# Kernel tuning notes

Hardware: AMD Instinct MI355X
Metric: run time of the kernel (lower is better)

Reference implementation:

```python
import jax, jax.numpy as jnp
import numpy as np

N_NODES = 32768
N_EDGES = 196608
N_GRAPHS = 256
DEG = 6
HID = 128
RVD = 16
EMB = HID - RVD   # atom/bond embedding dim = hidden - random_vec_dim
VOCAB = 128
TGT = 256
DEPTH = 5
N_AGG = 4         # mean, max, min, std
N_SC = 3          # identity, amplification, attenuation
EPS = 1e-5


def setup_inputs() -> dict:
    key = jax.random.key(0)
    ks = jax.random.split(key, 12)

    def g(i, shape, scale=0.05):
        return jax.random.normal(ks[i], shape, dtype=jnp.float32) * scale

    return {
        "atom_feats": jax.random.randint(ks[0], (N_NODES, 9), 0, 100),
        "bond_feats": jax.random.randint(ks[1], (N_EDGES, 3), 0, 4),
        "src": jax.random.randint(ks[2], (N_EDGES,), 0, N_NODES),
        # every node receives exactly DEG messages (DGL reduce requires in-edges)
        "dst": jnp.repeat(jnp.arange(N_NODES), DEG),
        "graph_ids": jnp.repeat(jnp.arange(N_GRAPHS), N_NODES // N_GRAPHS),
        "n_graphs": N_GRAPHS,
        "rand_x": jax.random.normal(ks[3], (N_NODES, RVD), dtype=jnp.float32),   # std=1.0
        "rand_edge": jax.random.normal(ks[4], (N_EDGES, RVD), dtype=jnp.float32),
        "atom_emb": g(5, (9, VOCAB, EMB)),
        "bond_emb": g(6, (3, VOCAB, EMB)),
        "pre_W": g(7, (DEPTH, 3 * HID, HID)),
        "pre_b": jnp.zeros((DEPTH, HID), jnp.float32),
        "post_W": g(8, (DEPTH, (N_AGG * N_SC + 1) * HID, HID)),
        "post_b": jnp.zeros((DEPTH, HID), jnp.float32),
        "ro_W1": g(9, (3 * HID, HID)),
        "ro_b1": jnp.zeros((HID,), jnp.float32),
        "ro_W2": g(10, (HID, TGT)),
        "ro_b2": jnp.zeros((TGT,), jnp.float32),
    }


def reference(atom_feats, bond_feats, src, dst, graph_ids, n_graphs,
              rand_x, rand_edge, atom_emb, bond_emb,
              pre_W, pre_b, post_W, post_b, ro_W1, ro_b1, ro_W2, ro_b2):
    n = atom_feats.shape[0]
    # OGB-style encoders: sum of per-column embeddings, then concat random vec
    h = jnp.concatenate([atom_emb[jnp.arange(9), atom_feats].sum(1), rand_x], -1)   # [N, HID]
    ef = jnp.concatenate([bond_emb[jnp.arange(3), bond_feats].sum(1), rand_edge], -1)  # [E, HID]

    deg = jax.ops.segment_sum(jnp.ones((dst.shape[0],), h.dtype), dst, n)
    degc = jnp.maximum(deg, 1.0)[:, None]
    logD = jnp.log(deg + 1.0)[:, None]                 # avg_d['log'] = 1.0
    inv_logD = jnp.where(logD > 0, 1.0 / jnp.maximum(logD, EPS), 0.0)

    def layer(hc, p):
        pW, pb, qW, qb = p
        # pretrans MLP on [src_feat, dst_feat, edge_feat]; last_activation = activation (relu)
        z = jnp.concatenate([hc[src], hc[dst], ef], -1)          # [E, 3*HID]
        e = jax.nn.relu(z @ pW + pb)                             # [E, HID]
        s = jax.ops.segment_sum(e, dst, n)
        mean = s / degc
        mean_sq = jax.ops.segment_sum(e * e, dst, n) / degc
        mx = jax.ops.segment_max(e, dst, n)
        mn = jax.ops.segment_min(e, dst, n)
        std = jnp.sqrt(jax.nn.relu(mean_sq - mean * mean) + EPS)
        agg = jnp.concatenate([mean, mx, mn, std], -1)           # [N, 4*HID]
        scaled = jnp.concatenate([agg, agg * logD, agg * inv_logD], -1)  # [N, 12*HID]
        h_new = jnp.concatenate([hc, scaled], -1) @ qW + qb + hc  # posttrans (linear) + residual
        return h_new, None

    h, _ = jax.lax.scan(layer, h, (pre_W, pre_b, post_W, post_b))

    # multi-aggregator readout: mean, sum, max per graph
    cnt = jnp.maximum(jax.ops.segment_sum(jnp.ones((n,), h.dtype), graph_ids, n_graphs), 1.0)[:, None]
    gsum = jax.ops.segment_sum(h, graph_ids, n_graphs)
    gmax = jax.ops.segment_max(h, graph_ids, n_graphs)
    r = jnp.concatenate([gsum / cnt, gsum, gmax], -1)            # [G, 3*HID]
    return jax.nn.relu(r @ ro_W1 + ro_b1) @ ro_W2 + ro_b2        # [G, TGT]
```

## Files before the change

### kernel.cpp

```cpp
#include <hip/hip_runtime.h>
#include <hip/hip_bf16.h>

#define N_NODES 32768
#define N_EDGES 196608
#define N_GRAPHS 256
#define DEG 6
#define HID 128
#define RVD 16
#define EMB 112
#define VOCAB 128
#define TGT 256
#define DEPTH 5

#define LOG7 1.9459101090932196f
#define ILOG7 0.5138983423697507f

typedef __hip_bfloat16 bf16;
using frag_ab = __attribute__((ext_vector_type(8))) short;
using frag_cd = __attribute__((ext_vector_type(4))) float;

static __device__ __forceinline__ float b2f(bf16 x) { return __bfloat162float(x); }
static __device__ __forceinline__ bf16  f2b(float x) { return __float2bfloat16(x); }
static __device__ __forceinline__ short f2s(float x) {
    bf16 b = __float2bfloat16(x);
    return *reinterpret_cast<short*>(&b);
}
static __device__ __forceinline__ float us2f(unsigned short u) {
    unsigned int x = ((unsigned int)u) << 16;
    return __uint_as_float(x);
}
static __device__ __forceinline__ unsigned short f2us(float x) {
    bf16 b = __float2bfloat16(x);
    return *reinterpret_cast<unsigned short*>(&b);
}

#define PB_ENC  16384
#define PB_WB   (PB_ENC + 640)
#define PB_WC   (PB_WB + 1600)
#define PB_WR   (PB_WC + 80)
#define PB_CODE (PB_WR + 768)
#define PB_T    (PB_CODE + 320)

__global__ __launch_bounds__(256) void prep_k(const int* __restrict__ af, const float* __restrict__ rx,
                                              const float* __restrict__ aemb, bf16* __restrict__ h,
                                              const float* __restrict__ preW, const float* __restrict__ preB,
                                              const float* __restrict__ postW,
                                              const int* __restrict__ bfeat, const float* __restrict__ bemb,
                                              bf16* __restrict__ wb, bf16* __restrict__ wc,
                                              bf16* __restrict__ wrB, unsigned char* __restrict__ codeA,
                                              bf16* __restrict__ Tb) {
    int blk = blockIdx.x, tid = threadIdx.x;
    if (blk < PB_ENC) {
        int v = blk * 2 + (tid >> 7), c = tid & 127;
        float val;
        if (c < EMB) {
            val = 0.f;
            #pragma unroll
            for (int i = 0; i < 9; ++i) {
                int f = af[v * 9 + i];
                val += aemb[(i * VOCAB + f) * EMB + c];
            }
        } else {
            val = rx[v * RVD + (c - EMB)];
        }
        h[(size_t)v * HID + c] = f2b(val);
    } else if (blk < PB_WB) {
        int idx = (blk - PB_ENC) * 256 + tid;
        if (idx < DEPTH * 32768) {
            int j = idx & 7, L = (idx >> 3) & 63, nt = (idx >> 9) & 15, ks = (idx >> 13) & 3, l = idx >> 15;
            int k = ks * 32 + ((L >> 4) * 8) + j;
            int n = nt * 16 + (L & 15);
            const float* W = preW + (size_t)l * 384 * 128;
            float v = (n < 128) ? W[k * 128 + n] : W[(128 + k) * 128 + (n - 128)];
            wb[idx] = f2b(v);
        }
    } else if (blk < PB_WC) {
        int idx = (blk - PB_WB) * 256 + tid;
        if (idx < DEPTH * 81920) {
            int j = idx & 7, L = (idx >> 3) & 63, nt = (idx >> 9) & 7;
            int t = idx >> 12;
            int ks = t % 20, l = t / 20;
            int k = ks * 32 + ((L >> 4) * 8) + j;
            int n = nt * 16 + (L & 15);
            const float* W = postW + (size_t)l * 1664 * 128;
            float v;
            if (k < 128) {
                v = W[k * 128 + n];
            } else {
                int jj = k - 128;
                v = W[(128 + jj) * 128 + n] + LOG7 * W[(640 + jj) * 128 + n] + ILOG7 * W[(1152 + jj) * 128 + n];
            }
            wc[idx] = f2b(v);
        }
    } else if (blk < PB_WR) {
        int idx = (blk - PB_WC) * 256 + tid;
        if (idx < DEPTH * 4096) {
            int j = idx & 7, L = (idx >> 3) & 63, nt = (idx >> 9) & 7, l = idx >> 12;
            int k = ((L >> 4) * 8) + j;
            int n = nt * 16 + (L & 15);
            float v = (k < 16) ? preW[(size_t)l * 384 * 128 + (368 + k) * 128 + n] : 0.f;
            wrB[idx] = f2b(v);
        }
    } else if (blk < PB_CODE) {
        int e = (blk - PB_WR) * 256 + tid;
        if (e < N_EDGES)
            codeA[e] = (unsigned char)(bfeat[e * 3] | (bfeat[e * 3 + 1] << 2) | (bfeat[e * 3 + 2] << 4));
    } else {
        if (tid < 128) {
            int t = blk - PB_CODE;
            int l = t >> 6, cd = t & 63, c = tid;
            int f0 = cd & 3, f1 = (cd >> 2) & 3, f2 = cd >> 4;
            const float* W = preW + (size_t)l * 384 * 128 + 256 * 128;
            float acc = preB[l * 128 + c];
            #pragma unroll 4
            for (int k = 0; k < EMB; ++k) {
                float bsk = bemb[(0 * VOCAB + f0) * EMB + k]
                          + bemb[(1 * VOCAB + f1) * EMB + k]
                          + bemb[(2 * VOCAB + f2) * EMB + k];
                acc += bsk * W[k * 128 + c];
            }
            Tb[(size_t)(l * 64 + cd) * 128 + c] = f2b(acc);
        }
    }
}

__global__ __launch_bounds__(256) void gemm_z12(const bf16* __restrict__ A,
                                                const bf16* __restrict__ Bp,
                                                bf16* __restrict__ C) {
    int lane = threadIdx.x & 63;
    int wave = threadIdx.x >> 6;
    int m = lane & 15, quad = lane >> 4;
    int row0 = blockIdx.x * 64 + wave * 16;

    frag_cd acc[16];
    #pragma unroll
    for (int nt = 0; nt < 16; ++nt)
        #pragma unroll
        for (int i = 0; i < 4; ++i) acc[nt][i] = 0.f;

    const frag_ab* Bf = (const frag_ab*)Bp;
    const bf16* arow = A + (size_t)(row0 + m) * 128;
    #pragma unroll
    for (int ks = 0; ks < 4; ++ks) {
        frag_ab a = *(const frag_ab*)(arow + ks * 32 + quad * 8);
        #pragma unroll
        for (int nt = 0; nt < 16; ++nt) {
            frag_ab b = Bf[(ks * 16 + nt) * 64 + lane];
            acc[nt] = __builtin_amdgcn_mfma_f32_16x16x32_bf16(a, b, acc[nt], 0, 0, 0);
        }
    }
    #pragma unroll
    for (int nt = 0; nt < 16; ++nt) {
        int col = nt * 16 + m;
        #pragma unroll
        for (int r = 0; r < 4; ++r) {
            int row = row0 + quad * 4 + r;
            C[(size_t)row * 256 + col] = f2b(acc[nt][r]);
        }
    }
}

__global__ __launch_bounds__(512) void layer_k(bf16* __restrict__ h,
                                               const bf16* __restrict__ aggc,
                                               const bf16* __restrict__ Bp,
                                               const float* __restrict__ bias,
                                               const bf16* __restrict__ Bn,
                                               bf16* __restrict__ z12) {
    __shared__ __align__(16) bf16 newh[64 * 136];
    int lane = threadIdx.x & 63;
    int wave = threadIdx.x >> 6;
    int rt = wave & 3;
    int nh = wave >> 2;
    int m = lane & 15, quad = lane >> 4;
    int row0 = blockIdx.x * 64;
    int rowA = row0 + rt * 16 + m;

    frag_cd acc[4];
    #pragma unroll
    for (int nt = 0; nt < 4; ++nt)
        #pragma unroll
        for (int i = 0; i < 4; ++i) acc[nt][i] = 0.f;

    const frag_ab* Bf = (const frag_ab*)Bp;
    const bf16* arow = h + (size_t)rowA * 128;
    #pragma unroll
    for (int ks = 0; ks < 4; ++ks) {
        frag_ab a = *(const frag_ab*)(arow + ks * 32 + quad * 8);
        #pragma unroll
        for (int nt = 0; nt < 4; ++nt) {
            frag_ab b = Bf[(ks * 8 + nh * 4 + nt) * 64 + lane];
            acc[nt] = __builtin_amdgcn_mfma_f32_16x16x32_bf16(a, b, acc[nt], 0, 0, 0);
        }
    }
    const bf16* grow = aggc + (size_t)rowA * 512;
    #pragma unroll
    for (int ks = 0; ks < 16; ++ks) {
        frag_ab a = *(const frag_ab*)(grow + ks * 32 + quad * 8);
        #pragma unroll
        for (int nt = 0; nt < 4; ++nt) {
            frag_ab b = Bf[((4 + ks) * 8 + nh * 4 + nt) * 64 + lane];
            acc[nt] = __builtin_amdgcn_mfma_f32_16x16x32_bf16(a, b, acc[nt], 0, 0, 0);
        }
    }

    __syncthreads();

    #pragma unroll
    for (int nt = 0; nt < 4; ++nt) {
        int col = nh * 64 + nt * 16 + m;
        float bs_ = bias[col];
        #pragma unroll
        for (int r = 0; r < 4; ++r) {
            int lr = rt * 16 + quad * 4 + r;
            int row = row0 + lr;
            float nv = acc[nt][r] + bs_ + b2f(h[(size_t)row * HID + col]);
            bf16 bv = f2b(nv);
            h[(size_t)row * HID + col] = bv;
            newh[lr * 136 + col] = bv;
        }
    }

    if (Bn) {
        __syncthreads();
        const frag_ab* Bf2 = (const frag_ab*)Bn;
        frag_cd a2[8];
        #pragma unroll
        for (int nt = 0; nt < 8; ++nt)
            #pragma unroll
            for (int i = 0; i < 4; ++i) a2[nt][i] = 0.f;
        #pragma unroll
        for (int ks = 0; ks < 4; ++ks) {
            frag_ab a = *(const frag_ab*)&newh[(rt * 16 + m) * 136 + ks * 32 + quad * 8];
            #pragma unroll
            for (int nt = 0; nt < 8; ++nt) {
                frag_ab b = Bf2[(ks * 16 + nh * 8 + nt) * 64 + lane];
                a2[nt] = __builtin_amdgcn_mfma_f32_16x16x32_bf16(a, b, a2[nt], 0, 0, 0);
            }
        }
        #pragma unroll
        for (int nt = 0; nt < 8; ++nt) {
            int col = nh * 128 + nt * 16 + m;
            #pragma unroll
            for (int r = 0; r < 4; ++r) {
                int row = row0 + rt * 16 + quad * 4 + r;
                z12[(size_t)row * 256 + col] = f2b(a2[nt][r]);
            }
        }
    }
}

__global__ __launch_bounds__(256) void fused_agg(const bf16* __restrict__ Z12,
                                                 const int* __restrict__ src,
                                                 const unsigned char* __restrict__ code,
                                                 const float* __restrict__ rand_edge,
                                                 const bf16* __restrict__ Tb,
                                                 const bf16* __restrict__ WrB,
                                                 bf16* __restrict__ aggc) {
    __shared__ __align__(16) float rdot[48 * 130];
    int tid = threadIdx.x;
    int lane = tid & 63, wave = tid >> 6;
    int xb = blockIdx.x & 7, tb = blockIdx.x >> 3;
    int w = xb + 8 * (tb >> 3);
    int bv = w * 64 + (tb & 7) * 8;

    if (wave < 3) {
        int m = lane & 15, quad = lane >> 4;
        frag_ab a;
        if (quad < 2) {
            const float4* rp = (const float4*)(rand_edge
                + (size_t)(bv * 6 + wave * 16 + m) * 16 + quad * 8);
            float4 A = rp[0], B = rp[1];
            a[0] = f2s(A.x); a[1] = f2s(A.y); a[2] = f2s(A.z); a[3] = f2s(A.w);
            a[4] = f2s(B.x); a[5] = f2s(B.y); a[6] = f2s(B.z); a[7] = f2s(B.w);
        } else {
            #pragma unroll
            for (int j = 0; j < 8; ++j) a[j] = 0;
        }
        const frag_ab* Bf = (const frag_ab*)WrB;
        #pragma unroll
        for (int nt = 0; nt < 8; ++nt) {
            frag_cd acc;
            #pragma unroll
            for (int i = 0; i < 4; ++i) acc[i] = 0.f;
            acc = __builtin_amdgcn_mfma_f32_16x16x32_bf16(a, Bf[nt * 64 + lane], acc, 0, 0, 0);
            #pragma unroll
            for (int r = 0; r < 4; ++r)
                rdot[(wave * 16 + quad * 4 + r) * 130 + nt * 16 + m] = acc[r];
        }
    }
    __syncthreads();

    const unsigned short* Zu = (const unsigned short*)Z12;
    const unsigned short* Tu = (const unsigned short*)Tb;
    unsigned short* Au = (unsigned short*)aggc;
    int c = lane * 2;
    int g = wave;

    #pragma unroll
    for (int i = 0; i < 2; ++i) {
        int nb = g * 2 + i;
        int v = bv + nb;
        ushort2 z2u = *(const ushort2*)(Zu + (size_t)v * 256 + 128 + c);
        float z2a = us2f(z2u.x), z2b = us2f(z2u.y);
        const int2* sp = (const int2*)(src + v * 6);
        int2 s01 = sp[0], s23 = sp[1], s45 = sp[2];
        const unsigned short* cp = (const unsigned short*)(code + v * 6);
        unsigned short c01 = cp[0], c23 = cp[1], c45 = cp[2];
        int svs[6] = { s01.x, s01.y, s23.x, s23.y, s45.x, s45.y };
        int cds[6] = { c01 & 255, c01 >> 8, c23 & 255, c23 >> 8, c45 & 255, c45 >> 8 };
        ushort2 z1u[6], tvu[6];
        #pragma unroll
        for (int j = 0; j < 6; ++j) z1u[j] = *(const ushort2*)(Zu + (size_t)svs[j] * 256 + c);
        #pragma unroll
        for (int j = 0; j < 6; ++j) tvu[j] = *(const ushort2*)(Tu + cds[j] * 128 + c);
        float sa = 0.f, ssa = 0.f, mxa = -1e30f, mna = 1e30f;
        float sb = 0.f, ssb = 0.f, mxb = -1e30f, mnb = 1e30f;
        #pragma unroll
        for (int j = 0; j < 6; ++j) {
            const float2 rd = *(const float2*)(rdot + ((nb * 6 + j) * 130) + c);
            float va = us2f(z1u[j].x) + z2a + us2f(tvu[j].x) + rd.x;
            float vb = us2f(z1u[j].y) + z2b + us2f(tvu[j].y) + rd.y;
            va = fmaxf(va, 0.f);
            vb = fmaxf(vb, 0.f);
            sa += va; ssa += va * va; mxa = fmaxf(mxa, va); mna = fminf(mna, va);
            sb += vb; ssb += vb * vb; mxb = fmaxf(mxb, vb); mnb = fminf(mnb, vb);
        }
        float meana = sa * (1.f / 6.f), meanb = sb * (1.f / 6.f);
        float msqa = ssa * (1.f / 6.f), msqb = ssb * (1.f / 6.f);
        float sda = sqrtf(fmaxf(msqa - meana * meana, 0.f) + 1e-5f);
        float sdb = sqrtf(fmaxf(msqb - meanb * meanb, 0.f) + 1e-5f);
        size_t base = (size_t)v * 512 + c;
        *(ushort2*)(Au + base)       = make_ushort2(f2us(meana), f2us(meanb));
        *(ushort2*)(Au + base + 128) = make_ushort2(f2us(mxa),  f2us(mxb));
        *(ushort2*)(Au + base + 256) = make_ushort2(f2us(mna),  f2us(mnb));
        *(ushort2*)(Au + base + 384) = make_ushort2(f2us(sda),  f2us(sdb));
    }
}

__global__ __launch_bounds__(128) void readout(const bf16* __restrict__ h, const float* __restrict__ W1,
                                               const float* __restrict__ b1, const float* __restrict__ W2,
                                               const float* __restrict__ b2, float* __restrict__ out) {
    __shared__ float r[384];
    __shared__ float y1[128];
    int g = blockIdx.x, c = threadIdx.x;
    float s = 0.f, mx = -1e30f;
    for (int v = 0; v < 128; ++v) {
        float hv = b2f(h[((size_t)g * 128 + v) * HID + c]);
        s += hv; mx = fmaxf(mx, hv);
    }
    r[c] = s * (1.f / 128.f);
    r[128 + c] = s;
    r[256 + c] = mx;
    __syncthreads();
    float a1 = b1[c];
    for (int k = 0; k < 384; ++k) a1 += r[k] * W1[k * 128 + c];
    y1[c] = fmaxf(a1, 0.f);
    __syncthreads();
    #pragma unroll
    for (int o = 0; o < 2; ++o) {
        int t = c + o * 128;
        float a2 = b2[t];
        for (int k = 0; k < 128; ++k) a2 += y1[k] * W2[k * 256 + t];
        out[(size_t)g * 256 + t] = a2;
    }
}

extern "C" void kernel_launch(void* const* d_in, const int* in_sizes, int n_in,
                              void* d_out, int out_size, void* d_ws, size_t ws_size,
                              hipStream_t stream) {
    const int*   atom_feats = (const int*)d_in[0];
    const int*   bond_feats = (const int*)d_in[1];
    const int*   src        = (const int*)d_in[2];
    const float* rand_x     = (const float*)d_in[6];
    const float* rand_edge  = (const float*)d_in[7];
    const float* atom_emb   = (const float*)d_in[8];
    const float* bond_emb   = (const float*)d_in[9];
    const float* pre_W      = (const float*)d_in[10];
    const float* pre_b      = (const float*)d_in[11];
    const float* post_W     = (const float*)d_in[12];
    const float* post_b     = (const float*)d_in[13];
    const float* ro_W1      = (const float*)d_in[14];
    const float* ro_b1      = (const float*)d_in[15];
    const float* ro_W2      = (const float*)d_in[16];
    const float* ro_b2      = (const float*)d_in[17];

    char* p = (char*)d_ws;
    auto alloc = [&](size_t bytes) {
        char* r = p;
        p += (bytes + 255) & ~(size_t)255;
        return r;
    };
    bf16*  h    = (bf16*) alloc((size_t)N_NODES * HID * 2);
    bf16*  z12  = (bf16*) alloc((size_t)N_NODES * 256 * 2);
    bf16*  aggc = (bf16*) alloc((size_t)N_NODES * 512 * 2);
    bf16*  wb   = (bf16*) alloc((size_t)DEPTH * 32768 * 2);
    bf16*  wc   = (bf16*) alloc((size_t)DEPTH * 81920 * 2);
    bf16*  wrB  = (bf16*) alloc((size_t)DEPTH * 4096 * 2);
    bf16*  Tb   = (bf16*) alloc((size_t)DEPTH * 64 * 128 * 2);
    unsigned char* code = (unsigned char*)alloc(N_EDGES);

    prep_k<<<PB_T, 256, 0, stream>>>(atom_feats, rand_x, atom_emb, h,
                                     pre_W, pre_b, post_W,
                                     bond_feats, bond_emb,
                                     wb, wc, wrB, code, Tb);

    gemm_z12<<<N_NODES / 64, 256, 0, stream>>>(h, wb, z12);

    for (int l = 0; l < DEPTH; ++l) {
        fused_agg<<<N_NODES / 8, 256, 0, stream>>>(
            z12, src, code, rand_edge,
            Tb + (size_t)l * 8192,
            wrB + (size_t)l * 4096, aggc);
        const bf16* wbn = (l + 1 < DEPTH) ? (wb + (size_t)(l + 1) * 32768) : nullptr;
        layer_k<<<N_NODES / 64, 512, 0, stream>>>(
            h, aggc, wc + (size_t)l * 81920, post_b + l * HID, wbn, z12);
    }

    readout<<<N_GRAPHS, 128, 0, stream>>>(h, ro_W1, ro_b1, ro_W2, ro_b2, (float*)d_out);
}
```

Measured before the change: 379.4 us.

## Fuse edge aggregation into layer kernel with LDS aggregates and ping-pong Z buffers

Merges the per-layer aggregation kernel and the post-transform GEMM kernel into one kernel. The 64x512 aggregate tile is kept in shared memory rather than written to and read back from a global aggc buffer, and the rdot values are stored as bf16. Z12 is double-buffered so the next layer's Z can be written while other blocks still gather the current one. This removes global aggregate traffic and one launch per layer. In exchange it adds about 80KB of LDS per block and runs aggregation serially over 8 sub-batches with barriers, which may lower occupancy and latency hiding for the gathers.

```diff
diff --git a/kernel.cpp b/kernel.cpp
--- a/kernel.cpp
+++ b/kernel.cpp
@@ -160,19 +160,101 @@
     }
 }
 
-__global__ __launch_bounds__(512) void layer_k(bf16* __restrict__ h,
-                                               const bf16* __restrict__ aggc,
-                                               const bf16* __restrict__ Bp,
-                                               const float* __restrict__ bias,
-                                               const bf16* __restrict__ Bn,
-                                               bf16* __restrict__ z12) {
-    __shared__ __align__(16) bf16 newh[64 * 136];
-    int lane = threadIdx.x & 63;
-    int wave = threadIdx.x >> 6;
-    int rt = wave & 3;
-    int nh = wave >> 2;
+__global__ __launch_bounds__(512, 4) void fused_layer(bf16* __restrict__ h,
+                                                      const bf16* __restrict__ Zcur,
+                                                      const int* __restrict__ src,
+                                                      const unsigned char* __restrict__ code,
+                                                      const float* __restrict__ rand_edge,
+                                                      const bf16* __restrict__ Tb,
+                                                      const bf16* __restrict__ WrB,
+                                                      const bf16* __restrict__ Bp,
+                                                      const float* __restrict__ bias,
+                                                      const bf16* __restrict__ Bn,
+                                                      bf16* __restrict__ Znext) {
+    __shared__ __align__(16) bf16 agg_lds[64 * 520];
+    __shared__ __align__(16) bf16 rdot[48 * 136];
+
+    int tid = threadIdx.x;
+    int lane = tid & 63, wave = tid >> 6;
     int m = lane & 15, quad = lane >> 4;
     int row0 = blockIdx.x * 64;
+
+    const unsigned short* Zu = (const unsigned short*)Zcur;
+    const unsigned short* Tu = (const unsigned short*)Tb;
+    const unsigned short* Ru = (const unsigned short*)rdot;
+    unsigned short* Ag = (unsigned short*)agg_lds;
+    int c = lane * 2;
+
+    for (int r = 0; r < 8; ++r) {
+        int bv = row0 + r * 8;
+        if (wave < 3) {
+            frag_ab a;
+            if (quad < 2) {
+                const float4* rp = (const float4*)(rand_edge
+                    + (size_t)(bv * 6 + wave * 16 + m) * 16 + quad * 8);
+                float4 A = rp[0], B = rp[1];
+                a[0] = f2s(A.x); a[1] = f2s(A.y); a[2] = f2s(A.z); a[3] = f2s(A.w);
+                a[4] = f2s(B.x); a[5] = f2s(B.y); a[6] = f2s(B.z); a[7] = f2s(B.w);
+            } else {
+                #pragma unroll
+                for (int j = 0; j < 8; ++j) a[j] = 0;
+            }
+            const frag_ab* Bf = (const frag_ab*)WrB;
+            #pragma unroll
+            for (int nt = 0; nt < 8; ++nt) {
+                frag_cd acc;
+                #pragma unroll
+                for (int i = 0; i < 4; ++i) acc[i] = 0.f;
+                acc = __builtin_amdgcn_mfma_f32_16x16x32_bf16(a, Bf[nt * 64 + lane], acc, 0, 0, 0);
+                #pragma unroll
+                for (int rr = 0; rr < 4; ++rr)
+                    rdot[(wave * 16 + quad * 4 + rr) * 136 + nt * 16 + m] = f2b(acc[rr]);
+            }
+        }
+        __syncthreads();
+        {
+            int nb = wave;
+            int v = bv + nb;
+            ushort2 z2u = *(const ushort2*)(Zu + (size_t)v * 256 + 128 + c);
+            float z2a = us2f(z2u.x), z2b = us2f(z2u.y);
+            const int2* sp = (const int2*)(src + v * 6);
+            int2 s01 = sp[0], s23 = sp[1], s45 = sp[2];
+            const unsigned short* cp = (const unsigned short*)(code + v * 6);
+            unsigned short c01 = cp[0], c23 = cp[1], c45 = cp[2];
+            int svs[6] = { s01.x, s01.y, s23.x, s23.y, s45.x, s45.y };
+            int cds[6] = { c01 & 255, c01 >> 8, c23 & 255, c23 >> 8, c45 & 255, c45 >> 8 };
+            ushort2 z1u[6], tvu[6];
+            #pragma unroll
+            for (int j = 0; j < 6; ++j) z1u[j] = *(const ushort2*)(Zu + (size_t)svs[j] * 256 + c);
+            #pragma unroll
+            for (int j = 0; j < 6; ++j) tvu[j] = *(const ushort2*)(Tu + cds[j] * 128 + c);
+            float sa = 0.f, ssa = 0.f, mxa = -1e30f, mna = 1e30f;
+            float sb = 0.f, ssb = 0.f, mxb = -1e30f, mnb = 1e30f;
+            #pragma unroll
+            for (int j = 0; j < 6; ++j) {
+                ushort2 rdu = *(const ushort2*)(Ru + (nb * 6 + j) * 136 + c);
+                float va = us2f(z1u[j].x) + z2a + us2f(tvu[j].x) + us2f(rdu.x);
+                float vb = us2f(z1u[j].y) + z2b + us2f(tvu[j].y) + us2f(rdu.y);
+                va = fmaxf(va, 0.f);
+                vb = fmaxf(vb, 0.f);
+                sa += va; ssa += va * va; mxa = fmaxf(mxa, va); mna = fminf(mna, va);
+                sb += vb; ssb += vb * vb; mxb = fmaxf(mxb, vb); mnb = fminf(mnb, vb);
+            }
+            float meana = sa * (1.f / 6.f), meanb = sb * (1.f / 6.f);
+            float msqa = ssa * (1.f / 6.f), msqb = ssb * (1.f / 6.f);
+            float sda = sqrtf(fmaxf(msqa - meana * meana, 0.f) + 1e-5f);
+            float sdb = sqrtf(fmaxf(msqb - meanb * meanb, 0.f) + 1e-5f);
+            int lrow = r * 8 + nb;
+            size_t base = (size_t)lrow * 520 + c;
+            *(ushort2*)(Ag + base)       = make_ushort2(f2us(meana), f2us(meanb));
+            *(ushort2*)(Ag + base + 128) = make_ushort2(f2us(mxa),  f2us(mxb));
+            *(ushort2*)(Ag + base + 256) = make_ushort2(f2us(mna),  f2us(mnb));
+            *(ushort2*)(Ag + base + 384) = make_ushort2(f2us(sda),  f2us(sdb));
+        }
+        __syncthreads();
+    }
+
+    int rt = wave & 3, nh = wave >> 2;
     int rowA = row0 + rt * 16 + m;
 
     frag_cd acc[4];
@@ -192,7 +274,7 @@
             acc[nt] = __builtin_amdgcn_mfma_f32_16x16x32_bf16(a, b, acc[nt], 0, 0, 0);
         }
     }
-    const bf16* grow = aggc + (size_t)rowA * 512;
+    const bf16* grow = agg_lds + (size_t)(rt * 16 + m) * 520;
     #pragma unroll
     for (int ks = 0; ks < 16; ++ks) {
         frag_ab a = *(const frag_ab*)(grow + ks * 32 + quad * 8);
@@ -205,18 +287,19 @@
 
     __syncthreads();
 
+    bf16* newh = agg_lds;
     #pragma unroll
     for (int nt = 0; nt < 4; ++nt) {
         int col = nh * 64 + nt * 16 + m;
         float bs_ = bias[col];
         #pragma unroll
-        for (int r = 0; r < 4; ++r) {
-            int lr = rt * 16 + quad * 4 + r;
+        for (int r2 = 0; r2 < 4; ++r2) {
+            int lr = rt * 16 + quad * 4 + r2;
             int row = row0 + lr;
-            float nv = acc[nt][r] + bs_ + b2f(h[(size_t)row * HID + col]);
-            bf16 bv = f2b(nv);
-            h[(size_t)row * HID + col] = bv;
-            newh[lr * 136 + col] = bv;
+            float nv = acc[nt][r2] + bs_ + b2f(h[(size_t)row * HID + col]);
+            bf16 bv2 = f2b(nv);
+            h[(size_t)row * HID + col] = bv2;
+            newh[lr * 136 + col] = bv2;
         }
     }
 
@@ -241,99 +324,11 @@
         for (int nt = 0; nt < 8; ++nt) {
             int col = nh * 128 + nt * 16 + m;
             #pragma unroll
-            for (int r = 0; r < 4; ++r) {
-                int row = row0 + rt * 16 + quad * 4 + r;
-                z12[(size_t)row * 256 + col] = f2b(a2[nt][r]);
-            }
-        }
-    }
-}
-
-__global__ __launch_bounds__(256) void fused_agg(const bf16* __restrict__ Z12,
-                                                 const int* __restrict__ src,
-                                                 const unsigned char* __restrict__ code,
-                                                 const float* __restrict__ rand_edge,
-                                                 const bf16* __restrict__ Tb,
-                                                 const bf16* __restrict__ WrB,
-                                                 bf16* __restrict__ aggc) {
-    __shared__ __align__(16) float rdot[48 * 130];
-    int tid = threadIdx.x;
-    int lane = tid & 63, wave = tid >> 6;
-    int xb = blockIdx.x & 7, tb = blockIdx.x >> 3;
-    int w = xb + 8 * (tb >> 3);
-    int bv = w * 64 + (tb & 7) * 8;
-
-    if (wave < 3) {
-        int m = lane & 15, quad = lane >> 4;
-        frag_ab a;
-        if (quad < 2) {
-            const float4* rp = (const float4*)(rand_edge
-                + (size_t)(bv * 6 + wave * 16 + m) * 16 + quad * 8);
-            float4 A = rp[0], B = rp[1];
-            a[0] = f2s(A.x); a[1] = f2s(A.y); a[2] = f2s(A.z); a[3] = f2s(A.w);
-            a[4] = f2s(B.x); a[5] = f2s(B.y); a[6] = f2s(B.z); a[7] = f2s(B.w);
-        } else {
-            #pragma unroll
-            for (int j = 0; j < 8; ++j) a[j] = 0;
-        }
-        const frag_ab* Bf = (const frag_ab*)WrB;
-        #pragma unroll
-        for (int nt = 0; nt < 8; ++nt) {
-            frag_cd acc;
-            #pragma unroll
-            for (int i = 0; i < 4; ++i) acc[i] = 0.f;
-            acc = __builtin_amdgcn_mfma_f32_16x16x32_bf16(a, Bf[nt * 64 + lane], acc, 0, 0, 0);
-            #pragma unroll
-            for (int r = 0; r < 4; ++r)
-                rdot[(wave * 16 + quad * 4 + r) * 130 + nt * 16 + m] = acc[r];
-        }
-    }
-    __syncthreads();
-
-    const unsigned short* Zu = (const unsigned short*)Z12;
-    const unsigned short* Tu = (const unsigned short*)Tb;
-    unsigned short* Au = (unsigned short*)aggc;
-    int c = lane * 2;
-    int g = wave;
-
-    #pragma unroll
-    for (int i = 0; i < 2; ++i) {
-        int nb = g * 2 + i;
-        int v = bv + nb;
-        ushort2 z2u = *(const ushort2*)(Zu + (size_t)v * 256 + 128 + c);
-        float z2a = us2f(z2u.x), z2b = us2f(z2u.y);
-        const int2* sp = (const int2*)(src + v * 6);
-        int2 s01 = sp[0], s23 = sp[1], s45 = sp[2];
-        const unsigned short* cp = (const unsigned short*)(code + v * 6);
-        unsigned short c01 = cp[0], c23 = cp[1], c45 = cp[2];
-        int svs[6] = { s01.x, s01.y, s23.x, s23.y, s45.x, s45.y };
-        int cds[6] = { c01 & 255, c01 >> 8, c23 & 255, c23 >> 8, c45 & 255, c45 >> 8 };
-        ushort2 z1u[6], tvu[6];
-        #pragma unroll
-        for (int j = 0; j < 6; ++j) z1u[j] = *(const ushort2*)(Zu + (size_t)svs[j] * 256 + c);
-        #pragma unroll
-        for (int j = 0; j < 6; ++j) tvu[j] = *(const ushort2*)(Tu + cds[j] * 128 + c);
-        float sa = 0.f, ssa = 0.f, mxa = -1e30f, mna = 1e30f;
-        float sb = 0.f, ssb = 0.f, mxb = -1e30f, mnb = 1e30f;
-        #pragma unroll
-        for (int j = 0; j < 6; ++j) {
-            const float2 rd = *(const float2*)(rdot + ((nb * 6 + j) * 130) + c);
-            float va = us2f(z1u[j].x) + z2a + us2f(tvu[j].x) + rd.x;
-            float vb = us2f(z1u[j].y) + z2b + us2f(tvu[j].y) + rd.y;
-            va = fmaxf(va, 0.f);
-            vb = fmaxf(vb, 0.f);
-            sa += va; ssa += va * va; mxa = fmaxf(mxa, va); mna = fminf(mna, va);
-            sb += vb; ssb += vb * vb; mxb = fmaxf(mxb, vb); mnb = fminf(mnb, vb);
-        }
-        float meana = sa * (1.f / 6.f), meanb = sb * (1.f / 6.f);
-        float msqa = ssa * (1.f / 6.f), msqb = ssb * (1.f / 6.f);
-        float sda = sqrtf(fmaxf(msqa - meana * meana, 0.f) + 1e-5f);
-        float sdb = sqrtf(fmaxf(msqb - meanb * meanb, 0.f) + 1e-5f);
-        size_t base = (size_t)v * 512 + c;
-        *(ushort2*)(Au + base)       = make_ushort2(f2us(meana), f2us(meanb));
-        *(ushort2*)(Au + base + 128) = make_ushort2(f2us(mxa),  f2us(mxb));
-        *(ushort2*)(Au + base + 256) = make_ushort2(f2us(mna),  f2us(mnb));
-        *(ushort2*)(Au + base + 384) = make_ushort2(f2us(sda),  f2us(sdb));
+            for (int r2 = 0; r2 < 4; ++r2) {
+                int row = row0 + rt * 16 + quad * 4 + r2;
+                Znext[(size_t)row * 256 + col] = f2b(a2[nt][r2]);
+            }
+        }
     }
 }
 
@@ -391,8 +386,8 @@
         return r;
     };
     bf16*  h    = (bf16*) alloc((size_t)N_NODES * HID * 2);
-    bf16*  z12  = (bf16*) alloc((size_t)N_NODES * 256 * 2);
-    bf16*  aggc = (bf16*) alloc((size_t)N_NODES * 512 * 2);
+    bf16*  z12a = (bf16*) alloc((size_t)N_NODES * 256 * 2);
+    bf16*  z12b = (bf16*) alloc((size_t)N_NODES * 256 * 2);
     bf16*  wb   = (bf16*) alloc((size_t)DEPTH * 32768 * 2);
     bf16*  wc   = (bf16*) alloc((size_t)DEPTH * 81920 * 2);
     bf16*  wrB  = (bf16*) alloc((size_t)DEPTH * 4096 * 2);
@@ -404,16 +399,20 @@
                                      bond_feats, bond_emb,
                                      wb, wc, wrB, code, Tb);
 
-    gemm_z12<<<N_NODES / 64, 256, 0, stream>>>(h, wb, z12);
-
+    gemm_z12<<<N_NODES / 64, 256, 0, stream>>>(h, wb, z12a);
+
+    bf16* zc = z12a;
+    bf16* zn = z12b;
     for (int l = 0; l < DEPTH; ++l) {
-        fused_agg<<<N_NODES / 8, 256, 0, stream>>>(
-            z12, src, code, rand_edge,
+        const bf16* wbn = (l + 1 < DEPTH) ? (wb + (size_t)(l + 1) * 32768) : nullptr;
+        fused_layer<<<N_NODES / 64, 512, 0, stream>>>(
+            h, zc, src, code, rand_edge,
             Tb + (size_t)l * 8192,
-            wrB + (size_t)l * 4096, aggc);
-        const bf16* wbn = (l + 1 < DEPTH) ? (wb + (size_t)(l + 1) * 32768) : nullptr;
-        layer_k<<<N_NODES / 64, 512, 0, stream>>>(
-            h, aggc, wc + (size_t)l * 81920, post_b + l * HID, wbn, z12);
+            wrB + (size_t)l * 4096,
+            wc + (size_t)l * 81920,
+            post_b + l * HID,
+            wbn, zn);
+        bf16* t = zc; zc = zn; zn = t;
     }
 
     readout<<<N_GRAPHS, 128, 0, stream>>>(h, ro_W1, ro_b1, ro_W2, ro_b2, (float*)d_out);
```

New measurement: 344.3 us. 9.2% less time.
